# Kernel tuning notes

Measured on AMD Instinct MI355X. Metric: run time of the kernel, lower is better.

## Reference

```python
import jax, jax.numpy as jnp
import numpy as np
from jax import lax


def setup_inputs() -> dict:
    key = jax.random.key(0)
    x = jax.random.normal(key, (4, 8192, 3), dtype=jnp.float32)
    return {"x": x, "k": 16}


def reference(x, k):
    p = x[..., :3]                                  # (B, N, 3)
    # Brute-force KNN: squared euclidean distances (B, N, N)
    sq = jnp.sum(p * p, axis=-1)                    # (B, N)
    d2 = sq[:, :, None] + sq[:, None, :] - 2.0 * jnp.einsum('bnd,bmd->bnm', p, p)
    _, idx = lax.top_k(-d2, k)                      # (B, N, k), nearest (incl. self)
    # Gather neighbors per batch
    neighbors = jax.vmap(lambda pts, ids: pts[ids])(p, idx)   # (B, N, k, 3)
    mean = jnp.mean(neighbors, axis=2, keepdims=True)          # (B, N, 1, 3)
    diff = neighbors - mean                                    # (B, N, k, 3)
    # cov = mean_k (diff diff^T) over neighbors -> (B, N, 3, 3)
    cov = jnp.einsum('bnki,bnkj->bnij', diff, diff) / k
    ev = jnp.linalg.eigvalsh(cov)                  # ascending: (B, N, 3)
    lambda0 = ev[..., 2]
    lambda1 = ev[..., 1]
    return lambda0 / lambda1
```

## Files before the change

### kernel.cpp

```cpp
#include <hip/hip_runtime.h>
#include <math.h>

#define NB 4
#define NP 8192
#define KK 16
#define QPB 64
#define NPTS (NB * NP)

#define TSAMP 1024
#define TTCH 128
#define BCH 1024
#define NBCH 8
#define CAP 62
#define SROW 66
#define SCH (64 * SROW + 2)
#define KCH 17
#define KQS (NBCH * KCH + 1)
#define PADKEY 0xFFFFFFFFFFFFFFFFull
#define TAU_MARGIN 2.5e-4f

#define CSWAP_DESC(a, b) { float _lo = fminf(a, b); float _hi = fmaxf(a, b); a = _hi; b = _lo; }
#define CSWAP_ASC(a, b)  { float _lo = fminf(a, b); float _hi = fmaxf(a, b); a = _lo; b = _hi; }

__device__ __forceinline__ float ref_sq(float x, float y, float z) {
  return __fadd_rn(__fadd_rn(__fmul_rn(x, x), __fmul_rn(y, y)), __fmul_rn(z, z));
}

__device__ __forceinline__ float ref_d2q(float qx, float qy, float qz, float sqq,
                                         float4 c) {
  float dot = __fadd_rn(__fadd_rn(__fmul_rn(qx, c.x), __fmul_rn(qy, c.y)),
                        __fmul_rn(qz, c.z));
  float s = __fadd_rn(sqq, c.w);
  return __fmaf_rn(-2.0f, dot, s);
}

__device__ __forceinline__ float fast_d2(float qx, float qy, float qz, float sqq,
                                         float4 c) {
  float dot = __fmaf_rn(qz, c.z, __fmaf_rn(qy, c.y, __fmul_rn(qx, c.x)));
  float s = __fadd_rn(sqq, c.w);
  return __fmaf_rn(-2.0f, dot, s);
}

__device__ __forceinline__ unsigned int ord_f32(float d) {
  unsigned int b = __float_as_uint(d);
  return b ^ ((b >> 31) ? 0xFFFFFFFFu : 0x80000000u);
}

__device__ __forceinline__ double eigen_ratio_tail(
    float cxx, float cyy, float czz, float cxy, float cxz, float cyz,
    float k1) {
  double a   = (double)__fmul_rn(cxx, k1), b = (double)__fmul_rn(cyy, k1);
  double c2  = (double)__fmul_rn(czz, k1);
  double dxy = (double)__fmul_rn(cxy, k1), exz = (double)__fmul_rn(cxz, k1);
  double fyz = (double)__fmul_rn(cyz, k1);
  double qm = (a + b + c2) / 3.0;
  double p1 = dxy * dxy + exz * exz + fyz * fyz;
  double aa = a - qm, bb = b - qm, cc = c2 - qm;
  double p2 = aa * aa + bb * bb + cc * cc + 2.0 * p1;
  if (p2 <= 0.0) return 1.0;
  double p  = sqrt(p2 / 6.0);
  double ip = 1.0 / p;
  double b00 = aa * ip, b11 = bb * ip, b22 = cc * ip;
  double b01 = dxy * ip, b02 = exz * ip, b12 = fyz * ip;
  double detB = b00 * (b11 * b22 - b12 * b12)
              - b01 * (b01 * b22 - b12 * b02)
              + b02 * (b01 * b12 - b11 * b02);
  double r = 0.5 * detB;
  r = fmin(1.0, fmax(-1.0, r));
  const double dcl = 2.0 * r;
  float phif = acosf((float)r) * (1.0f / 3.0f);
  double y0 = 2.0 * (double)cosf(phif);
  double y2 = 2.0 * (double)cosf(phif + 2.0943951f);
#pragma unroll
  for (int it = 0; it < 3; ++it) {
    double g0 = 3.0 * (y0 * y0 - 1.0);
    if (fabs(g0) > 1e-4) y0 -= (y0 * y0 * y0 - 3.0 * y0 - dcl) / g0;
    double g2 = 3.0 * (y2 * y2 - 1.0);
    if (fabs(g2) > 1e-4) y2 -= (y2 * y2 * y2 - 3.0 * y2 - dcl) / g2;
  }
  double e0 = qm + p * y0;
  double e2v = qm + p * y2;
  double e1 = 3.0 * qm - e0 - e2v;
  return e0 / e1;
}

__device__ __forceinline__ void topk_update(float bd[KK], float d[8]) {
  CSWAP_DESC(d[0], d[1]) CSWAP_DESC(d[2], d[3]) CSWAP_DESC(d[4], d[5]) CSWAP_DESC(d[6], d[7])
  CSWAP_DESC(d[0], d[2]) CSWAP_DESC(d[1], d[3]) CSWAP_DESC(d[4], d[6]) CSWAP_DESC(d[5], d[7])
  CSWAP_DESC(d[1], d[2]) CSWAP_DESC(d[5], d[6])
  CSWAP_DESC(d[0], d[4]) CSWAP_DESC(d[1], d[5]) CSWAP_DESC(d[2], d[6]) CSWAP_DESC(d[3], d[7])
  CSWAP_DESC(d[2], d[4]) CSWAP_DESC(d[3], d[5])
  CSWAP_DESC(d[1], d[2]) CSWAP_DESC(d[3], d[4]) CSWAP_DESC(d[5], d[6])
#pragma unroll
  for (int i = 0; i < 8; ++i) bd[8 + i] = fminf(bd[8 + i], d[i]);
#pragma unroll
  for (int i = 0; i < 8; ++i)  CSWAP_ASC(bd[i], bd[i + 8])
#pragma unroll
  for (int i = 0; i < 4; ++i)  CSWAP_ASC(bd[i], bd[i + 4])
#pragma unroll
  for (int i = 8; i < 12; ++i) CSWAP_ASC(bd[i], bd[i + 4])
#pragma unroll
  for (int g = 0; g < 4; ++g) {
    CSWAP_ASC(bd[4 * g + 0], bd[4 * g + 2]) CSWAP_ASC(bd[4 * g + 1], bd[4 * g + 3])
    CSWAP_ASC(bd[4 * g + 0], bd[4 * g + 1]) CSWAP_ASC(bd[4 * g + 2], bd[4 * g + 3])
  }
}

__global__ void prep_kernel(const float* __restrict__ x,
                            float4* __restrict__ cand) {
  int i = blockIdx.x * 256 + threadIdx.x;
  if (i < NPTS) {
    float px = x[3 * i + 0], py = x[3 * i + 1], pz = x[3 * i + 2];
    cand[i] = make_float4(px, py, pz, ref_sq(px, py, pz));
  }
}

__global__ __launch_bounds__(512, 4) void filter_select_kernel(
    const float4* __restrict__ cand, float* __restrict__ out) {
  extern __shared__ __align__(16) char smem[];
  float4* samp = (float4*)smem;
  float (*s_t)[64][17] = (float (*)[64][17])(smem + 16384);
  unsigned short* s_idx = (unsigned short*)smem;
  unsigned long long* keys = (unsigned long long*)smem;
  unsigned short* s_cnt = (unsigned short*)(smem + 70144);
  float* s_tau = (float*)(smem + 71168);

  const int tid   = threadIdx.x;
  const int lane  = tid & 63;
  const int w     = __builtin_amdgcn_readfirstlane(tid >> 6);
  const int group = blockIdx.x;
  const int batch = group >> 7;
  const int qbase = (group & 127) * QPB;
  const float4* __restrict__ Cb = cand + (size_t)batch * NP;

  const float4 q = Cb[qbase + lane];
  const float qx = q.x, qy = q.y, qz = q.z, sqq = q.w;

#pragma unroll
  for (int r = 0; r < TSAMP / 512; ++r)
    samp[r * 512 + tid] = Cb[r * 512 + tid];
  __syncthreads();

  {
    float bdA[KK], bdB[KK];
#pragma unroll
    for (int t = 0; t < KK; ++t) { bdA[t] = 3.4e38f; bdB[t] = 3.4e38f; }

    const int j0 = w * TTCH;
    for (int jj = 0; jj < TTCH; jj += 16) {
      float dA[8], dB[8];
      {
        const float4* xp = samp + (j0 + jj);
        float4 c[8];
#pragma unroll
        for (int u = 0; u < 8; ++u) c[u] = xp[u];
#pragma unroll
        for (int u = 0; u < 8; ++u) dA[u] = fast_d2(qx, qy, qz, sqq, c[u]);
      }
      {
        const float4* xp = samp + (j0 + jj + 8);
        float4 c[8];
#pragma unroll
        for (int u = 0; u < 8; ++u) c[u] = xp[u];
#pragma unroll
        for (int u = 0; u < 8; ++u) dB[u] = fast_d2(qx, qy, qz, sqq, c[u]);
      }
      topk_update(bdA, dA);
      topk_update(bdB, dB);
    }
    topk_update(bdA, &bdB[0]);
    topk_update(bdA, &bdB[8]);

#pragma unroll
    for (int t = 0; t < KK; ++t) s_t[w][lane][t] = bdA[t];
  }
  __syncthreads();

  if (w == 0) {
    float md[KK];
#pragma unroll
    for (int t = 0; t < KK; ++t) md[t] = s_t[0][lane][t];
#pragma unroll
    for (int s2 = 1; s2 < NBCH; ++s2) {
      float d[KK];
#pragma unroll
      for (int t = 0; t < KK; ++t) d[t] = s_t[s2][lane][t];
      topk_update(md, &d[0]);
      topk_update(md, &d[8]);
    }
    s_tau[lane] = md[KK - 1];
  }
  __syncthreads();

  {
    const int j0 = w * BCH;
    const float tau = s_tau[lane] + TAU_MARGIN;
    unsigned short* Srow = &s_idx[w * SCH + lane * SROW];
    int cnt = 0;
    for (int jj = 0; jj < BCH; jj += 16) {
      const float4* xp = Cb + (j0 + jj);
      float4 c[16];
#pragma unroll
      for (int u = 0; u < 16; ++u) c[u] = xp[u];
#pragma unroll
      for (int u = 0; u < 16; ++u) {
        float d = fast_d2(qx, qy, qz, sqq, c[u]);
        if (d <= tau) {
          if (cnt < CAP) Srow[1 + cnt] = (unsigned short)(j0 + jj + u);
          ++cnt;
        }
      }
    }
    s_cnt[w * 64 + lane] = (unsigned short)cnt;
  }
  __syncthreads();

  const int qlq = tid >> 3;
  const int pch = tid & 7;
  unsigned long long slots[KK];
#pragma unroll
  for (int t = 0; t < KK; ++t) slots[t] = PADKEY;
  {
    const float4 qq = Cb[qbase + qlq];
    const float q2x = qq.x, q2y = qq.y, q2z = qq.z, sq2 = qq.w;
    const unsigned short* row = &s_idx[pch * SCH + qlq * SROW + 1];
    int cnl = (int)s_cnt[pch * 64 + qlq];
    if (cnl > CAP) cnl = CAP;
    for (int e = 0; e < cnl; e += 8) {
      unsigned long long kv[8];
#pragma unroll
      for (int u = 0; u < 8; ++u) {
        const bool ok = (e + u) < cnl;
        const int j = ok ? (int)row[e + u] : 0;
        const float dd = ref_d2q(q2x, q2y, q2z, sq2, Cb[j]);
        kv[u] = ok ? ((((unsigned long long)ord_f32(dd)) << 32) |
                      (unsigned int)j)
                   : PADKEY;
      }
#pragma unroll
      for (int u = 0; u < 8; ++u) {
        const unsigned long long k = kv[u];
        if (k < slots[KK - 1]) {
#pragma unroll
          for (int t = KK - 1; t >= 1; --t) {
            unsigned long long lo =
                (slots[t] < k) ? slots[t] : k;
            slots[t] = (slots[t - 1] > lo) ? slots[t - 1] : lo;
          }
          slots[0] = (slots[0] < k) ? slots[0] : k;
        }
      }
    }
  }
  __syncthreads();

#pragma unroll
  for (int t = 0; t < KK; ++t)
    keys[qlq * KQS + pch * KCH + t] = slots[t];
  __syncthreads();

  if (tid < QPB) {
    const int ql = tid;
    const int qg = batch * NP + qbase + ql;
    const float4 qq = Cb[qbase + ql];
    const float q2x = qq.x, q2y = qq.y, q2z = qq.z, sq2 = qq.w;

    int total = 0;
    bool fs = false;
#pragma unroll
    for (int p = 0; p < NBCH; ++p) {
      const int c = (int)s_cnt[p * 64 + ql];
      if (c > CAP) fs = true;
      total += c;
    }
    if (total < KK) fs = true;

    int mjr[KK];
    if (!fs) {
      const unsigned long long* kq = keys + ql * KQS;
      int head[NBCH];
#pragma unroll
      for (int p = 0; p < NBCH; ++p) head[p] = 0;
#pragma unroll
      for (int t = 0; t < KK; ++t) {
        unsigned long long best = PADKEY;
        int bp = 0;
#pragma unroll
        for (int p = 0; p < NBCH; ++p) {
          const unsigned long long k =
              (head[p] < KK) ? kq[p * KCH + head[p]] : PADKEY;
          if (k < best) { best = k; bp = p; }
        }
        head[bp]++;
        mjr[t] = (int)(best & 0xFFFFull);
      }
    } else {
      float md[KK];
#pragma unroll
      for (int t = 0; t < KK; ++t) { md[t] = 3.4e38f; mjr[t] = 0; }
      for (int j = 0; j < NP; ++j) {
        float d = ref_d2q(q2x, q2y, q2z, sq2, Cb[j]);
        if (d < md[KK - 1]) {
          bool c0 = d < md[0];
#pragma unroll
          for (int t = KK - 1; t >= 1; --t) {
            bool cl = d < md[t];
            bool cp = d < md[t - 1];
            float nv = fmaxf(md[t - 1], fminf(md[t], d));
            mjr[t] = cl ? (cp ? mjr[t - 1] : j) : mjr[t];
            md[t] = nv;
          }
          mjr[0] = c0 ? j : mjr[0];
          md[0] = fminf(md[0], d);
        }
      }
    }

    float4 pts[KK];
#pragma unroll
    for (int s = 0; s < KK; ++s) pts[s] = Cb[mjr[s]];

    float sx = 0.f, sy = 0.f, sz = 0.f;
#pragma unroll
    for (int s = 0; s < KK; ++s) {
      sx = __fadd_rn(sx, pts[s].x);
      sy = __fadd_rn(sy, pts[s].y);
      sz = __fadd_rn(sz, pts[s].z);
    }
    const float k1 = 1.0f / KK;
    const float mx = sx * k1, my = sy * k1, mz = sz * k1;

    float cxx = 0.f, cxy = 0.f, cxz = 0.f, cyy = 0.f, cyz = 0.f, czz = 0.f;
#pragma unroll
    for (int s = 0; s < KK; ++s) {
      float dx = __fsub_rn(pts[s].x, mx);
      float dy = __fsub_rn(pts[s].y, my);
      float dz = __fsub_rn(pts[s].z, mz);
      cxx = __fadd_rn(cxx, __fmul_rn(dx, dx));
      cxy = __fadd_rn(cxy, __fmul_rn(dx, dy));
      cxz = __fadd_rn(cxz, __fmul_rn(dx, dz));
      cyy = __fadd_rn(cyy, __fmul_rn(dy, dy));
      cyz = __fadd_rn(cyz, __fmul_rn(dy, dz));
      czz = __fadd_rn(czz, __fmul_rn(dz, dz));
    }

    out[qg] = (float)eigen_ratio_tail(cxx, cyy, czz, cxy, cxz, cyz, k1);
  }
}

__global__ __launch_bounds__(512, 4) void knn_eigen_fallback(
    const float4* __restrict__ cand, float* __restrict__ out) {
  __shared__ unsigned short s_j[8][QPB][18];

  const int tid   = threadIdx.x;
  const int lane  = tid & 63;
  const int w     = __builtin_amdgcn_readfirstlane(tid >> 6);
  const int batch = blockIdx.x >> 7;
  const int qbase = (blockIdx.x & 127) * QPB;
  const int FCH   = NP / 8;

  const float4* __restrict__ Cb = cand + (size_t)batch * NP;

  const float4 q = Cb[qbase + lane];
  const float qx = q.x, qy = q.y, qz = q.z, sqq = q.w;

  float bd[KK];
#pragma unroll
  for (int t = 0; t < KK; ++t) bd[t] = 3.4e38f;

  const int j0 = w * FCH;
  for (int jj = 0; jj < FCH; jj += 8) {
    const float4* xp = Cb + (j0 + jj);
    float4 c[8];
#pragma unroll
    for (int u = 0; u < 8; ++u) c[u] = xp[u];
    float d[8];
#pragma unroll
    for (int u = 0; u < 8; ++u) d[u] = ref_d2q(qx, qy, qz, sqq, c[u]);
    topk_update(bd, d);
  }

  const float T = bd[KK - 1];
  int cnt = 0;
  for (int jj = 0; jj < FCH; jj += 8) {
    const float4* xp = Cb + (j0 + jj);
    float4 c[8];
#pragma unroll
    for (int u = 0; u < 8; ++u) c[u] = xp[u];
#pragma unroll
    for (int u = 0; u < 8; ++u) {
      float d = ref_d2q(qx, qy, qz, sqq, c[u]);
      if (d <= T && cnt < KK) {
        s_j[w][lane][cnt] = (unsigned short)(j0 + jj + u);
        cnt++;
      }
    }
  }
  __syncthreads();

  if (tid < QPB) {
    const float4 qq = Cb[qbase + tid];
    const float q2x = qq.x, q2y = qq.y, q2z = qq.z, sq2 = qq.w;
    float md[KK]; int mj[KK];
#pragma unroll
    for (int t = 0; t < KK; ++t) { md[t] = 3.4e38f; mj[t] = 0; }
    for (int cch = 0; cch < 8; ++cch) {
      const unsigned int* rowp = (const unsigned int*)&s_j[cch][tid][0];
#pragma unroll
      for (int sp = 0; sp < KK / 2; ++sp) {
        unsigned int pk = rowp[sp];
#pragma unroll
        for (int half = 0; half < 2; ++half) {
          int j = (half == 0) ? (int)(pk & 0xFFFFu) : (int)(pk >> 16);
          float d = ref_d2q(q2x, q2y, q2z, sq2, Cb[j]);
          if (d < md[KK - 1]) {
            bool c0 = d < md[0];
#pragma unroll
            for (int t = KK - 1; t >= 1; --t) {
              bool cl = d < md[t];
              bool cp = d < md[t - 1];
              float nv = fmaxf(md[t - 1], fminf(md[t], d));
              mj[t] = cl ? (cp ? mj[t - 1] : j) : mj[t];
              md[t] = nv;
            }
            mj[0] = c0 ? j : mj[0];
            md[0] = fminf(md[0], d);
          }
        }
      }
    }
    float sx = 0.f, sy = 0.f, sz = 0.f;
#pragma unroll
    for (int s = 0; s < KK; ++s) {
      float4 pp = Cb[mj[s]];
      sx = __fadd_rn(sx, pp.x);
      sy = __fadd_rn(sy, pp.y);
      sz = __fadd_rn(sz, pp.z);
    }
    const float k1 = 1.0f / KK;
    const float mx = sx * k1, my = sy * k1, mz = sz * k1;
    float cxx = 0.f, cxy = 0.f, cxz = 0.f, cyy = 0.f, cyz = 0.f, czz = 0.f;
#pragma unroll
    for (int s = 0; s < KK; ++s) {
      float4 pp = Cb[mj[s]];
      float dx = __fsub_rn(pp.x, mx);
      float dy = __fsub_rn(pp.y, my);
      float dz = __fsub_rn(pp.z, mz);
      cxx = __fadd_rn(cxx, __fmul_rn(dx, dx));
      cxy = __fadd_rn(cxy, __fmul_rn(dx, dy));
      cxz = __fadd_rn(cxz, __fmul_rn(dx, dz));
      cyy = __fadd_rn(cyy, __fmul_rn(dy, dy));
      cyz = __fadd_rn(cyz, __fmul_rn(dy, dz));
      czz = __fadd_rn(czz, __fmul_rn(dz, dz));
    }
    out[(size_t)batch * NP + qbase + tid] =
        (float)eigen_ratio_tail(cxx, cyy, czz, cxy, cxz, cyz, k1);
  }
}

extern "C" void kernel_launch(void* const* d_in, const int* in_sizes, int n_in,
                              void* d_out, int out_size, void* d_ws, size_t ws_size,
                              hipStream_t stream) {
  const float* x = (const float*)d_in[0];
  float* out = (float*)d_out;
  float4* cand = (float4*)d_ws;
  const size_t need = (size_t)NPTS * sizeof(float4);

  prep_kernel<<<dim3(NPTS / 256), dim3(256), 0, stream>>>(x, cand);
  if (ws_size >= need) {
    const size_t fs_lds = 71424;
    filter_select_kernel<<<dim3(512), dim3(512), fs_lds, stream>>>(cand, out);
  } else {
    knn_eigen_fallback<<<dim3(NPTS / QPB), dim3(512), 0, stream>>>(cand, out);
  }
}
```

Before: 184.7 us.

## Drop prep kernel and read packed xyz directly in filter-select kernel

Removes the prep kernel that expanded points to float4 with precomputed squared norms. The main kernel now reads the raw 3-float layout: sample tiles are loaded as float4 vectors into shared memory, and the scan loads 12 float4s per 16 points. The filter passes use a difference-based distance, and the exact pass recomputes norms on the fly. This saves a launch and reduces global traffic, at the cost of extra arithmetic and unaligned strided scalar gathers in the exact and gather stages.

```diff
diff --git a/kernel.cpp b/kernel.cpp
--- a/kernel.cpp
+++ b/kernel.cpp
@@ -26,19 +26,19 @@
   return __fadd_rn(__fadd_rn(__fmul_rn(x, x), __fmul_rn(y, y)), __fmul_rn(z, z));
 }
 
-__device__ __forceinline__ float ref_d2q(float qx, float qy, float qz, float sqq,
-                                         float4 c) {
-  float dot = __fadd_rn(__fadd_rn(__fmul_rn(qx, c.x), __fmul_rn(qy, c.y)),
-                        __fmul_rn(qz, c.z));
-  float s = __fadd_rn(sqq, c.w);
+__device__ __forceinline__ float ref_d2(float qx, float qy, float qz, float sqq,
+                                        float cx, float cy, float cz) {
+  float sqc = ref_sq(cx, cy, cz);
+  float dot = __fadd_rn(__fadd_rn(__fmul_rn(qx, cx), __fmul_rn(qy, cy)),
+                        __fmul_rn(qz, cz));
+  float s = __fadd_rn(sqq, sqc);
   return __fmaf_rn(-2.0f, dot, s);
 }
 
-__device__ __forceinline__ float fast_d2(float qx, float qy, float qz, float sqq,
-                                         float4 c) {
-  float dot = __fmaf_rn(qz, c.z, __fmaf_rn(qy, c.y, __fmul_rn(qx, c.x)));
-  float s = __fadd_rn(sqq, c.w);
-  return __fmaf_rn(-2.0f, dot, s);
+__device__ __forceinline__ float diff_d2(float qx, float qy, float qz,
+                                         float cx, float cy, float cz) {
+  float dx = cx - qx, dy = cy - qy, dz = cz - qz;
+  return __fmaf_rn(dz, dz, __fmaf_rn(dy, dy, dx * dx));
 }
 
 __device__ __forceinline__ unsigned int ord_f32(float d) {
@@ -106,17 +106,8 @@
   }
 }
 
-__global__ void prep_kernel(const float* __restrict__ x,
-                            float4* __restrict__ cand) {
-  int i = blockIdx.x * 256 + threadIdx.x;
-  if (i < NPTS) {
-    float px = x[3 * i + 0], py = x[3 * i + 1], pz = x[3 * i + 2];
-    cand[i] = make_float4(px, py, pz, ref_sq(px, py, pz));
-  }
-}
-
 __global__ __launch_bounds__(512, 4) void filter_select_kernel(
-    const float4* __restrict__ cand, float* __restrict__ out) {
+    const float* __restrict__ x, float* __restrict__ out) {
   extern __shared__ __align__(16) char smem[];
   float4* samp = (float4*)smem;
   float (*s_t)[64][17] = (float (*)[64][17])(smem + 16384);
@@ -131,17 +122,25 @@
   const int group = blockIdx.x;
   const int batch = group >> 7;
   const int qbase = (group & 127) * QPB;
-  const float4* __restrict__ Cb = cand + (size_t)batch * NP;
-
-  const float4 q = Cb[qbase + lane];
-  const float qx = q.x, qy = q.y, qz = q.z, sqq = q.w;
-
-#pragma unroll
-  for (int r = 0; r < TSAMP / 512; ++r)
-    samp[r * 512 + tid] = Cb[r * 512 + tid];
-  __syncthreads();
+  const float* __restrict__ Xb = x + (size_t)batch * NP * 3;
+
+  const float qx = Xb[3 * (qbase + lane) + 0];
+  const float qy = Xb[3 * (qbase + lane) + 1];
+  const float qz = Xb[3 * (qbase + lane) + 2];
+  const float sqq = ref_sq(qx, qy, qz);
 
   {
+    const float4* X4 = (const float4*)Xb;
+#pragma unroll
+    for (int r = 0; r < 2; ++r) {
+      const int idx = r * 512 + tid;
+      if (idx < (TSAMP * 3) / 4) samp[idx] = X4[idx];
+    }
+  }
+  __syncthreads();
+
+  {
+    const float* sf = (const float*)samp;
     float bdA[KK], bdB[KK];
 #pragma unroll
     for (int t = 0; t < KK; ++t) { bdA[t] = 3.4e38f; bdB[t] = 3.4e38f; }
@@ -149,21 +148,15 @@
     const int j0 = w * TTCH;
     for (int jj = 0; jj < TTCH; jj += 16) {
       float dA[8], dB[8];
-      {
-        const float4* xp = samp + (j0 + jj);
-        float4 c[8];
-#pragma unroll
-        for (int u = 0; u < 8; ++u) c[u] = xp[u];
-#pragma unroll
-        for (int u = 0; u < 8; ++u) dA[u] = fast_d2(qx, qy, qz, sqq, c[u]);
-      }
-      {
-        const float4* xp = samp + (j0 + jj + 8);
-        float4 c[8];
-#pragma unroll
-        for (int u = 0; u < 8; ++u) c[u] = xp[u];
-#pragma unroll
-        for (int u = 0; u < 8; ++u) dB[u] = fast_d2(qx, qy, qz, sqq, c[u]);
+#pragma unroll
+      for (int u = 0; u < 8; ++u) {
+        const int j = 3 * (j0 + jj + u);
+        dA[u] = diff_d2(qx, qy, qz, sf[j], sf[j + 1], sf[j + 2]);
+      }
+#pragma unroll
+      for (int u = 0; u < 8; ++u) {
+        const int j = 3 * (j0 + jj + 8 + u);
+        dB[u] = diff_d2(qx, qy, qz, sf[j], sf[j + 1], sf[j + 2]);
       }
       topk_update(bdA, dA);
       topk_update(bdB, dB);
@@ -198,13 +191,14 @@
     unsigned short* Srow = &s_idx[w * SCH + lane * SROW];
     int cnt = 0;
     for (int jj = 0; jj < BCH; jj += 16) {
-      const float4* xp = Cb + (j0 + jj);
-      float4 c[16];
-#pragma unroll
-      for (int u = 0; u < 16; ++u) c[u] = xp[u];
+      const float4* xp = (const float4*)(Xb + (size_t)(j0 + jj) * 3);
+      float4 cv[12];
+#pragma unroll
+      for (int u = 0; u < 12; ++u) cv[u] = xp[u];
+      const float* f = (const float*)cv;
 #pragma unroll
       for (int u = 0; u < 16; ++u) {
-        float d = fast_d2(qx, qy, qz, sqq, c[u]);
+        float d = diff_d2(qx, qy, qz, f[3 * u], f[3 * u + 1], f[3 * u + 2]);
         if (d <= tau) {
           if (cnt < CAP) Srow[1 + cnt] = (unsigned short)(j0 + jj + u);
           ++cnt;
@@ -221,8 +215,10 @@
 #pragma unroll
   for (int t = 0; t < KK; ++t) slots[t] = PADKEY;
   {
-    const float4 qq = Cb[qbase + qlq];
-    const float q2x = qq.x, q2y = qq.y, q2z = qq.z, sq2 = qq.w;
+    const float q2x = Xb[3 * (qbase + qlq) + 0];
+    const float q2y = Xb[3 * (qbase + qlq) + 1];
+    const float q2z = Xb[3 * (qbase + qlq) + 2];
+    const float sq2 = ref_sq(q2x, q2y, q2z);
     const unsigned short* row = &s_idx[pch * SCH + qlq * SROW + 1];
     int cnl = (int)s_cnt[pch * 64 + qlq];
     if (cnl > CAP) cnl = CAP;
@@ -232,7 +228,8 @@
       for (int u = 0; u < 8; ++u) {
         const bool ok = (e + u) < cnl;
         const int j = ok ? (int)row[e + u] : 0;
-        const float dd = ref_d2q(q2x, q2y, q2z, sq2, Cb[j]);
+        const float cx = Xb[3 * j], cy = Xb[3 * j + 1], cz = Xb[3 * j + 2];
+        const float dd = ref_d2(q2x, q2y, q2z, sq2, cx, cy, cz);
         kv[u] = ok ? ((((unsigned long long)ord_f32(dd)) << 32) |
                       (unsigned int)j)
                    : PADKEY;
@@ -262,8 +259,10 @@
   if (tid < QPB) {
     const int ql = tid;
     const int qg = batch * NP + qbase + ql;
-    const float4 qq = Cb[qbase + ql];
-    const float q2x = qq.x, q2y = qq.y, q2z = qq.z, sq2 = qq.w;
+    const float q2x = Xb[3 * (qbase + ql) + 0];
+    const float q2y = Xb[3 * (qbase + ql) + 1];
+    const float q2z = Xb[3 * (qbase + ql) + 2];
+    const float sq2 = ref_sq(q2x, q2y, q2z);
 
     int total = 0;
     bool fs = false;
@@ -299,7 +298,8 @@
 #pragma unroll
       for (int t = 0; t < KK; ++t) { md[t] = 3.4e38f; mjr[t] = 0; }
       for (int j = 0; j < NP; ++j) {
-        float d = ref_d2q(q2x, q2y, q2z, sq2, Cb[j]);
+        float d = ref_d2(q2x, q2y, q2z, sq2,
+                         Xb[3 * j], Xb[3 * j + 1], Xb[3 * j + 2]);
         if (d < md[KK - 1]) {
           bool c0 = d < md[0];
 #pragma unroll
@@ -316,16 +316,20 @@
       }
     }
 
-    float4 pts[KK];
-#pragma unroll
-    for (int s = 0; s < KK; ++s) pts[s] = Cb[mjr[s]];
+    float px[KK], py[KK], pz[KK];
+#pragma unroll
+    for (int s = 0; s < KK; ++s) {
+      px[s] = Xb[3 * mjr[s]];
+      py[s] = Xb[3 * mjr[s] + 1];
+      pz[s] = Xb[3 * mjr[s] + 2];
+    }
 
     float sx = 0.f, sy = 0.f, sz = 0.f;
 #pragma unroll
     for (int s = 0; s < KK; ++s) {
-      sx = __fadd_rn(sx, pts[s].x);
-      sy = __fadd_rn(sy, pts[s].y);
-      sz = __fadd_rn(sz, pts[s].z);
+      sx = __fadd_rn(sx, px[s]);
+      sy = __fadd_rn(sy, py[s]);
+      sz = __fadd_rn(sz, pz[s]);
     }
     const float k1 = 1.0f / KK;
     const float mx = sx * k1, my = sy * k1, mz = sz * k1;
@@ -333,9 +337,9 @@
     float cxx = 0.f, cxy = 0.f, cxz = 0.f, cyy = 0.f, cyz = 0.f, czz = 0.f;
 #pragma unroll
     for (int s = 0; s < KK; ++s) {
-      float dx = __fsub_rn(pts[s].x, mx);
-      float dy = __fsub_rn(pts[s].y, my);
-      float dz = __fsub_rn(pts[s].z, mz);
+      float dx = __fsub_rn(px[s], mx);
+      float dy = __fsub_rn(py[s], my);
+      float dz = __fsub_rn(pz[s], mz);
       cxx = __fadd_rn(cxx, __fmul_rn(dx, dx));
       cxy = __fadd_rn(cxy, __fmul_rn(dx, dy));
       cxz = __fadd_rn(cxz, __fmul_rn(dx, dz));
@@ -348,129 +352,11 @@
   }
 }
 
-__global__ __launch_bounds__(512, 4) void knn_eigen_fallback(
-    const float4* __restrict__ cand, float* __restrict__ out) {
-  __shared__ unsigned short s_j[8][QPB][18];
-
-  const int tid   = threadIdx.x;
-  const int lane  = tid & 63;
-  const int w     = __builtin_amdgcn_readfirstlane(tid >> 6);
-  const int batch = blockIdx.x >> 7;
-  const int qbase = (blockIdx.x & 127) * QPB;
-  const int FCH   = NP / 8;
-
-  const float4* __restrict__ Cb = cand + (size_t)batch * NP;
-
-  const float4 q = Cb[qbase + lane];
-  const float qx = q.x, qy = q.y, qz = q.z, sqq = q.w;
-
-  float bd[KK];
-#pragma unroll
-  for (int t = 0; t < KK; ++t) bd[t] = 3.4e38f;
-
-  const int j0 = w * FCH;
-  for (int jj = 0; jj < FCH; jj += 8) {
-    const float4* xp = Cb + (j0 + jj);
-    float4 c[8];
-#pragma unroll
-    for (int u = 0; u < 8; ++u) c[u] = xp[u];
-    float d[8];
-#pragma unroll
-    for (int u = 0; u < 8; ++u) d[u] = ref_d2q(qx, qy, qz, sqq, c[u]);
-    topk_update(bd, d);
-  }
-
-  const float T = bd[KK - 1];
-  int cnt = 0;
-  for (int jj = 0; jj < FCH; jj += 8) {
-    const float4* xp = Cb + (j0 + jj);
-    float4 c[8];
-#pragma unroll
-    for (int u = 0; u < 8; ++u) c[u] = xp[u];
-#pragma unroll
-    for (int u = 0; u < 8; ++u) {
-      float d = ref_d2q(qx, qy, qz, sqq, c[u]);
-      if (d <= T && cnt < KK) {
-        s_j[w][lane][cnt] = (unsigned short)(j0 + jj + u);
-        cnt++;
-      }
-    }
-  }
-  __syncthreads();
-
-  if (tid < QPB) {
-    const float4 qq = Cb[qbase + tid];
-    const float q2x = qq.x, q2y = qq.y, q2z = qq.z, sq2 = qq.w;
-    float md[KK]; int mj[KK];
-#pragma unroll
-    for (int t = 0; t < KK; ++t) { md[t] = 3.4e38f; mj[t] = 0; }
-    for (int cch = 0; cch < 8; ++cch) {
-      const unsigned int* rowp = (const unsigned int*)&s_j[cch][tid][0];
-#pragma unroll
-      for (int sp = 0; sp < KK / 2; ++sp) {
-        unsigned int pk = rowp[sp];
-#pragma unroll
-        for (int half = 0; half < 2; ++half) {
-          int j = (half == 0) ? (int)(pk & 0xFFFFu) : (int)(pk >> 16);
-          float d = ref_d2q(q2x, q2y, q2z, sq2, Cb[j]);
-          if (d < md[KK - 1]) {
-            bool c0 = d < md[0];
-#pragma unroll
-            for (int t = KK - 1; t >= 1; --t) {
-              bool cl = d < md[t];
-              bool cp = d < md[t - 1];
-              float nv = fmaxf(md[t - 1], fminf(md[t], d));
-              mj[t] = cl ? (cp ? mj[t - 1] : j) : mj[t];
-              md[t] = nv;
-            }
-            mj[0] = c0 ? j : mj[0];
-            md[0] = fminf(md[0], d);
-          }
-        }
-      }
-    }
-    float sx = 0.f, sy = 0.f, sz = 0.f;
-#pragma unroll
-    for (int s = 0; s < KK; ++s) {
-      float4 pp = Cb[mj[s]];
-      sx = __fadd_rn(sx, pp.x);
-      sy = __fadd_rn(sy, pp.y);
-      sz = __fadd_rn(sz, pp.z);
-    }
-    const float k1 = 1.0f / KK;
-    const float mx = sx * k1, my = sy * k1, mz = sz * k1;
-    float cxx = 0.f, cxy = 0.f, cxz = 0.f, cyy = 0.f, cyz = 0.f, czz = 0.f;
-#pragma unroll
-    for (int s = 0; s < KK; ++s) {
-      float4 pp = Cb[mj[s]];
-      float dx = __fsub_rn(pp.x, mx);
-      float dy = __fsub_rn(pp.y, my);
-      float dz = __fsub_rn(pp.z, mz);
-      cxx = __fadd_rn(cxx, __fmul_rn(dx, dx));
-      cxy = __fadd_rn(cxy, __fmul_rn(dx, dy));
-      cxz = __fadd_rn(cxz, __fmul_rn(dx, dz));
-      cyy = __fadd_rn(cyy, __fmul_rn(dy, dy));
-      cyz = __fadd_rn(cyz, __fmul_rn(dy, dz));
-      czz = __fadd_rn(czz, __fmul_rn(dz, dz));
-    }
-    out[(size_t)batch * NP + qbase + tid] =
-        (float)eigen_ratio_tail(cxx, cyy, czz, cxy, cxz, cyz, k1);
-  }
-}
-
 extern "C" void kernel_launch(void* const* d_in, const int* in_sizes, int n_in,
                               void* d_out, int out_size, void* d_ws, size_t ws_size,
                               hipStream_t stream) {
   const float* x = (const float*)d_in[0];
   float* out = (float*)d_out;
-  float4* cand = (float4*)d_ws;
-  const size_t need = (size_t)NPTS * sizeof(float4);
-
-  prep_kernel<<<dim3(NPTS / 256), dim3(256), 0, stream>>>(x, cand);
-  if (ws_size >= need) {
-    const size_t fs_lds = 71424;
-    filter_select_kernel<<<dim3(512), dim3(512), fs_lds, stream>>>(cand, out);
-  } else {
-    knn_eigen_fallback<<<dim3(NPTS / QPB), dim3(512), 0, stream>>>(cand, out);
-  }
-}
+  const size_t fs_lds = 71424;
+  filter_select_kernel<<<dim3(512), dim3(512), fs_lds, stream>>>(x, out);
+}
```

Result: no change. 182.3 us (-1.3%).
